# Optimization experiments

Hardware: AMD Instinct MI355X
Metric: run time of the kernel (lower is better)

The kernel has to match this reference:

```python
import jax, jax.numpy as jnp
import numpy as np

ALPHA = 0.02      # LeakyReLU negative slope
N_GRAPHS = 128    # number of graphs in the batch (global_mean_pool segments)
NEG_INF = jnp.float32(-9e15)


def _gat_head(x, mask, W, a1, a2):
    # One GraphAttentionLayer (no dropout: eval mode).
    Wh = x @ W                                   # [N, h]
    f1 = Wh @ a1                                 # [N] = a[:h] . Wh_i
    f2 = Wh @ a2                                 # [N] = a[h:] . Wh_j
    e = jax.nn.leaky_relu(f1[:, None] + f2[None, :], negative_slope=ALPHA)  # [N, N]
    e = jnp.where(mask, e, NEG_INF)              # adjacency-masked logits
    att = jax.nn.softmax(e, axis=-1)             # row-wise over neighbors
    return att @ Wh                              # [N, h]


def reference(x, edge_index, batch, W_heads, a1_heads, a2_heads,
              W_out, a1_out, a2_out, W1, b1, W2, b2):
    N = x.shape[0]
    # adj[src, dst] = 1 via scatter, exactly as the torch code
    adj = jnp.zeros((N, N), dtype=jnp.float32).at[edge_index[0], edge_index[1]].set(1.0)
    mask = adj > 0
    # multi-head GAT, heads vmapped: [H, N, h]
    heads = jax.vmap(_gat_head, in_axes=(None, None, 0, 0, 0))(
        x, mask, W_heads, a1_heads, a2_heads)
    heads = jax.nn.elu(heads)                    # concat=True applies elu per head
    h = jnp.transpose(heads, (1, 0, 2)).reshape(N, -1)   # concat -> [N, H*h]
    out = jax.nn.elu(_gat_head(h, mask, W_out, a1_out, a2_out))  # out_att + outer elu
    # global mean pool over graphs
    seg_sum = jax.ops.segment_sum(out, batch, num_segments=N_GRAPHS)
    counts = jax.ops.segment_sum(jnp.ones((N,), jnp.float32), batch, num_segments=N_GRAPHS)
    pooled = seg_sum / jnp.maximum(counts, 1.0)[:, None]          # [G, att_out]
    # MLP head
    hid = jax.nn.relu(pooled @ W1 + b1)
    return hid @ W2 + b2                                          # [G, nout]


def setup_inputs() -> dict:
    key = jax.random.key(0)
    ks = jax.random.split(key, 12)
    N, F, H, HID, OUT, MLP, NOUT, E = 2048, 300, 20, 600, 1000, 1000, 768, 32768
    s = 0.05
    return {
        "x": jax.random.normal(ks[0], (N, F), jnp.float32),
        "edge_index": jax.random.randint(ks[1], (2, E), 0, N),
        "batch": jnp.sort(jax.random.randint(ks[2], (N,), 0, N_GRAPHS)),
        "W_heads": jax.random.normal(ks[3], (H, F, HID), jnp.float32) * s,
        "a1_heads": jax.random.normal(ks[4], (H, HID), jnp.float32) * s,
        "a2_heads": jax.random.normal(ks[5], (H, HID), jnp.float32) * s,
        "W_out": jax.random.normal(ks[6], (H * HID, OUT), jnp.float32) * 0.01,
        "a1_out": jax.random.normal(ks[7], (OUT,), jnp.float32) * s,
        "a2_out": jax.random.normal(ks[8], (OUT,), jnp.float32) * s,
        "W1": jax.random.normal(ks[9], (OUT, MLP), jnp.float32) * 0.03,
        "b1": jnp.zeros((MLP,), jnp.float32),
        "W2": jax.random.normal(ks[10], (MLP, NOUT), jnp.float32) * 0.03,
        "b2": jnp.zeros((NOUT,), jnp.float32),
    }
```

## Files before the change

kernel.cpp:

```cpp
#include <hip/hip_runtime.h>
#include <math.h>

#define NN   2048
#define FF   300
#define FP   320
#define NH   20
#define HHID 600
#define HP   640
#define HCAT (NH * HHID)
#define DOUT 1000
#define NPAD 1024
#define MLPD 1000
#define NOUTD 768
#define NE   32768
#define NG   128
#define CAP  160
#define KSPL 6
#define KCH  2016
#define PVC  16
#define PVR  16
#define PVU  47
#define PVHALF 750

typedef __attribute__((ext_vector_type(8))) short short8;
typedef __attribute__((ext_vector_type(4))) float f32x4;

__device__ __forceinline__ unsigned short f2bf(float f) {
  unsigned int u = __float_as_uint(f);
  u += 0x7fffu + ((u >> 16) & 1u);
  return (unsigned short)(u >> 16);
}
__device__ __forceinline__ float bf2f(unsigned short u) {
  return __uint_as_float(((unsigned int)u) << 16);
}
__device__ __forceinline__ void st_out(float* p, float v) { *p = v; }
__device__ __forceinline__ void st_out(unsigned short* p, float v) { *p = f2bf(v); }


__global__ void zero_words(unsigned int* __restrict__ p, int n) {
  int i = blockIdx.x * blockDim.x + threadIdx.x;
  int stride = gridDim.x * blockDim.x;
  for (; i < n; i += stride) p[i] = 0u;
}

__global__ void scatter_mask(const int* __restrict__ ei, unsigned char* __restrict__ mask) {
  int e = blockIdx.x * blockDim.x + threadIdx.x;
  if (e < NE) {
    int s = ei[e], d = ei[NE + e];
    mask[(size_t)s * NN + d] = 1;
  }
}

__global__ void build_csr(const unsigned char* __restrict__ mask,
                          int* __restrict__ nbr, int* __restrict__ deg) {
  int wave = threadIdx.x >> 6, lane = threadIdx.x & 63;
  int i = blockIdx.x * 4 + wave;
  if (i >= NN) return;
  const unsigned* roww = (const unsigned*)(mask + (size_t)i * NN);
  int cnt = 0;
  for (int c0 = 0; c0 < NN; c0 += 256) {
    unsigned word = roww[(c0 >> 2) + lane];
#pragma unroll
    for (int b = 0; b < 4; b++) {
      bool p = ((word >> (8 * b)) & 0xffu) != 0u;
      unsigned long long bal = __ballot(p);
      if (p) {
        int pos = cnt + (int)__popcll(bal & ((1ull << lane) - 1ull));
        if (pos < CAP) nbr[(size_t)i * CAP + pos] = c0 + lane * 4 + b;
      }
      cnt += (int)__popcll(bal);
    }
  }
  if (lane == 0) deg[i] = cnt < CAP ? cnt : CAP;
}


__global__ void w12_kernel(const float* __restrict__ W, const float* __restrict__ a1,
                           const float* __restrict__ a2,
                           float* __restrict__ w1, float* __restrict__ w2) {
  int k = blockIdx.x, hd = blockIdx.y, lane = threadIdx.x;
  const float* r = W + ((size_t)hd * FF + k) * HHID;
  const float* A1 = a1 + (size_t)hd * HHID;
  const float* A2 = a2 + (size_t)hd * HHID;
  float s1 = 0.f, s2 = 0.f;
  for (int c = lane; c < HHID; c += 64) {
    float w = r[c];
    s1 += w * A1[c];
    s2 += w * A2[c];
  }
  for (int off = 32; off; off >>= 1) {
    s1 += __shfl_down(s1, off);
    s2 += __shfl_down(s2, off);
  }
  if (lane == 0) { w1[(size_t)hd * FF + k] = s1; w2[(size_t)hd * FF + k] = s2; }
}

__global__ __launch_bounds__(256)
void f12x_kernel(const float* __restrict__ x, const float* __restrict__ w1,
                 const float* __restrict__ w2,
                 float* __restrict__ f1, float* __restrict__ f2) {
  __shared__ float xr[FF];
  int i = blockIdx.x, t = threadIdx.x;
  for (int c = t; c < FF; c += 256) xr[c] = x[(size_t)i * FF + c];
  __syncthreads();
  if (t < 2 * NH) {
    int hd = t >> 1;
    const float* wv = ((t & 1) ? w2 : w1) + (size_t)hd * FF;
    float s = 0.f;
    for (int k = 0; k < FF; k++) s += xr[k] * wv[k];
    ((t & 1) ? f2 : f1)[(size_t)hd * NN + i] = s;
  }
}

__global__ __launch_bounds__(256)
void csa_kernel(const float* __restrict__ xsum, const float* __restrict__ W,
                float* __restrict__ csa) {
  __shared__ float xs[FF];
  int hd = blockIdx.y, t = threadIdx.x;
  for (int k = t; k < FF; k += 256) xs[k] = xsum[k];
  __syncthreads();
  int c = blockIdx.x * 256 + t;
  if (c >= HHID) return;
  const float* Wp = W + (size_t)hd * FF * HHID + c;
  float s = 0.f;
  for (int k = 0; k < FF; k++) s += xs[k] * Wp[(size_t)k * HHID];
  csa[(size_t)hd * HHID + c] = s;
}


__global__ void f12_kernel(const float* __restrict__ Wh, int ldw, int h,
                           const float* __restrict__ a1, const float* __restrict__ a2,
                           int astride,
                           float* __restrict__ f1, float* __restrict__ f2) {
  int i = blockIdx.x, hd = blockIdx.y;
  int lane = threadIdx.x;
  const float* r = Wh + (size_t)i * ldw + (size_t)hd * h;
  const float* A1 = a1 + (size_t)hd * astride;
  const float* A2 = a2 + (size_t)hd * astride;
  float s1 = 0.f, s2 = 0.f;
  for (int c = lane; c < h; c += 64) {
    float w = r[c];
    s1 += w * A1[c];
    s2 += w * A2[c];
  }
  for (int off = 32; off; off >>= 1) {
    s1 += __shfl_down(s1, off);
    s2 += __shfl_down(s2, off);
  }
  if (lane == 0) { f1[(size_t)hd * NN + i] = s1; f2[(size_t)hd * NN + i] = s2; }
}

__global__ void f12_bf16(const unsigned short* __restrict__ Wh, int ldw, int h,
                         const float* __restrict__ a1, const float* __restrict__ a2,
                         int astride,
                         float* __restrict__ f1, float* __restrict__ f2) {
  int i = blockIdx.x, hd = blockIdx.y;
  int lane = threadIdx.x;
  const unsigned short* r = Wh + (size_t)i * ldw + (size_t)hd * h;
  const float* A1 = a1 + (size_t)hd * astride;
  const float* A2 = a2 + (size_t)hd * astride;
  float s1 = 0.f, s2 = 0.f;
  for (int c8 = lane; c8 < h / 8; c8 += 64) {
    short8 v = *(const short8*)(r + (size_t)c8 * 8);
#pragma unroll
    for (int j = 0; j < 8; j++) {
      float w = bf2f((unsigned short)v[j]);
      s1 += w * A1[c8 * 8 + j];
      s2 += w * A2[c8 * 8 + j];
    }
  }
  for (int off = 32; off; off >>= 1) {
    s1 += __shfl_down(s1, off);
    s2 += __shfl_down(s2, off);
  }
  if (lane == 0) { f1[(size_t)hd * NN + i] = s1; f2[(size_t)hd * NN + i] = s2; }
}

__global__ void colsum_kernel(const float* __restrict__ Wh, int ldw, int h,
                              float* __restrict__ cs) {
  int hd = blockIdx.y;
  int c = blockIdx.x * blockDim.x + threadIdx.x;
  if (c >= h) return;
  size_t off = (size_t)hd * h + c;
  float s = 0.f;
  for (int i = 0; i < NN; i++) s += Wh[(size_t)i * ldw + off];
  cs[(size_t)hd * h + c] = s;
}

__global__ void colsum_at_bf16(const unsigned short* __restrict__ Wh, int ld, int width,
                               float* __restrict__ cs) {
  int c = blockIdx.x * blockDim.x + threadIdx.x;
  if (c >= width) return;
  int r0 = blockIdx.y * 64;
  float s = 0.f;
  for (int i = r0; i < r0 + 64; i++) s += bf2f(Wh[(size_t)i * ld + c]);
  atomicAdd(&cs[c], s);
}

__global__ void colsum_at_f32(const float* __restrict__ Wh, int ld, int width,
                              float* __restrict__ cs) {
  int c = blockIdx.x * blockDim.x + threadIdx.x;
  if (c >= width) return;
  int r0 = blockIdx.y * 64;
  float s = 0.f;
  for (int i = r0; i < r0 + 64; i++) s += Wh[(size_t)i * ld + c];
  atomicAdd(&cs[c], s);
}


template <typename OT>
__global__ __launch_bounds__(256)
void spmm_att(const float* __restrict__ Wh, int ldw, int h,
              const float* __restrict__ f1, const float* __restrict__ f2,
              const int* __restrict__ nbr, const int* __restrict__ deg,
              const float* __restrict__ cs,
              OT* __restrict__ outp, int ldo) {
  __shared__ float att[CAP];
  __shared__ int   nb[CAP];
  __shared__ float red[256];
  int i = blockIdx.x, hd = blockIdx.y;
  int t = threadIdx.x;
  int d = deg[i];
  size_t hoff = (size_t)hd * h;
  if (d > 0) {
    float fi = f1[(size_t)hd * NN + i];
    const float* F2 = f2 + (size_t)hd * NN;
    float lmax = -INFINITY;
    for (int k = t; k < d; k += 256) {
      int j = nbr[(size_t)i * CAP + k];
      nb[k] = j;
      float e = fi + F2[j];
      e = e > 0.f ? e : 0.02f * e;
      att[k] = e;
      lmax = fmaxf(lmax, e);
    }
    red[t] = lmax; __syncthreads();
    for (int s = 128; s; s >>= 1) { if (t < s) red[t] = fmaxf(red[t], red[t + s]); __syncthreads(); }
    float m = red[0]; __syncthreads();
    float ls = 0.f;
    for (int k = t; k < d; k += 256) { float p = expf(att[k] - m); att[k] = p; ls += p; }
    red[t] = ls; __syncthreads();
    for (int s = 128; s; s >>= 1) { if (t < s) red[t] += red[t + s]; __syncthreads(); }
    float inv = 1.0f / red[0]; __syncthreads();
    for (int k = t; k < d; k += 256) att[k] *= inv;
    __syncthreads();
    for (int c = t; c < h; c += 256) {
      float s = 0.f;
      for (int k = 0; k < d; k++) s += att[k] * Wh[(size_t)nb[k] * ldw + hoff + c];
      s = s > 0.f ? s : (expf(s) - 1.0f);
      st_out(&outp[(size_t)i * ldo + hoff + c], s);
    }
  } else {
    const float inv = 1.0f / (float)NN;
    for (int c = t; c < h; c += 256) {
      float s = cs[hoff + c] * inv;
      s = s > 0.f ? s : (expf(s) - 1.0f);
      st_out(&outp[(size_t)i * ldo + hoff + c], s);
    }
  }
}

__global__ __launch_bounds__(256)
void att_pre(const float* __restrict__ f1, const float* __restrict__ f2,
             const int* __restrict__ nbr, const int* __restrict__ deg,
             float* __restrict__ att_c) {
  __shared__ int   nb_sh[CAP];
  __shared__ float att_sh[4][CAP];
  int i = blockIdx.x;
  int t = threadIdx.x, w = t >> 6, lane = t & 63;
  int hd = blockIdx.y * 4 + w;
  int d = deg[i];
  if (d == 0) return;
  for (int k = t; k < d; k += 256) nb_sh[k] = nbr[(size_t)i * CAP + k];
  __syncthreads();
  float fi = f1[(size_t)hd * NN + i];
  const float* F2 = f2 + (size_t)hd * NN;
  float lmax = -INFINITY;
  for (int k = lane; k < d; k += 64) {
    float e = fi + F2[nb_sh[k]];
    e = e > 0.f ? e : 0.02f * e;
    att_sh[w][k] = e;
    lmax = fmaxf(lmax, e);
  }
  for (int off = 32; off; off >>= 1) lmax = fmaxf(lmax, __shfl_xor(lmax, off));
  float ls = 0.f;
  for (int k = lane; k < d; k += 64) {
    float p = expf(att_sh[w][k] - lmax);
    att_sh[w][k] = p; ls += p;
  }
  for (int off = 32; off; off >>= 1) ls += __shfl_xor(ls, off);
  float inv = 1.0f / ls;
  float* ao = att_c + ((size_t)i * NH + hd) * CAP;
  for (int k = lane; k < d; k += 64) ao[k] = att_sh[w][k] * inv;
}

__global__ __launch_bounds__(256)
void spmm_pv(const unsigned short* __restrict__ Whb,
             const float* __restrict__ att_c,
             const int* __restrict__ nbr, const int* __restrict__ deg,
             const float* __restrict__ cs,
             unsigned short* __restrict__ outp,
             int ubase) {
  __shared__ int nb_sh[PVR][CAP];
  __shared__ int d_sh[PVR];
  int t = threadIdx.x;
  int r0 = blockIdx.y * PVR;
  int u0 = ubase + blockIdx.x * PVU;
  int ulim = ubase + PVHALF;
  int nu = (u0 + PVU <= ulim) ? PVU : (ulim - u0);
  if (t < PVR) d_sh[t] = deg[r0 + t];
  for (int q = t; q < PVR * CAP; q += 256) {
    int r = q / CAP, k = q - r * CAP;
    nb_sh[r][k] = nbr[(size_t)(r0 + r) * CAP + k];
  }
  __syncthreads();
  const float invn = 1.0f / (float)NN;
  int total = PVR * nu;
  for (int q = t; q < total; q += 256) {
    int r = q / nu, u = q - r * nu;
    int i = r0 + r;
    int gu = u0 + u;
    int hd = gu / (HHID / 8);
    int d = d_sh[r];
    const unsigned short* base = Whb + (size_t)gu * 8;
    unsigned short o8[8];
    if (d > 0) {
      const float* av = att_c + ((size_t)i * NH + hd) * CAP;
      float a8[8] = {};
      for (int k = 0; k < d; k++) {
        float a = av[k];
        short8 v = *(const short8*)(base + (size_t)nb_sh[r][k] * HCAT);
#pragma unroll
        for (int j = 0; j < 8; j++) a8[j] += a * bf2f((unsigned short)v[j]);
      }
#pragma unroll
      for (int j = 0; j < 8; j++) {
        float s = a8[j];
        s = s > 0.f ? s : (expf(s) - 1.0f);
        o8[j] = f2bf(s);
      }
    } else {
#pragma unroll
      for (int j = 0; j < 8; j++) {
        float s = cs[(size_t)gu * 8 + j] * invn;
        s = s > 0.f ? s : (expf(s) - 1.0f);
        o8[j] = f2bf(s);
      }
    }
    *(short8*)(outp + (size_t)i * HCAT + (size_t)gu * 8) = *(const short8*)o8;
  }
}

__global__ __launch_bounds__(128)
void spmm_att_o(const unsigned short* __restrict__ Wh,
                const float* __restrict__ f1, const float* __restrict__ f2,
                const int* __restrict__ nbr, const int* __restrict__ deg,
                const float* __restrict__ cs,
                float* __restrict__ outp) {
  __shared__ int   nb_sh[CAP];
  __shared__ float att_sh[CAP];
  __shared__ float red[128];
  int i = blockIdx.x, t = threadIdx.x;
  int d = deg[i];
  if (d > 0) {
    float fi = f1[i];
    float lmax = -INFINITY;
    for (int k = t; k < d; k += 128) {
      int j = nbr[(size_t)i * CAP + k];
      nb_sh[k] = j;
      float e = fi + f2[j];
      e = e > 0.f ? e : 0.02f * e;
      att_sh[k] = e;
      lmax = fmaxf(lmax, e);
    }
    red[t] = lmax; __syncthreads();
    for (int s = 64; s; s >>= 1) { if (t < s) red[t] = fmaxf(red[t], red[t + s]); __syncthreads(); }
    float m = red[0]; __syncthreads();
    float ls = 0.f;
    for (int k = t; k < d; k += 128) { float p = expf(att_sh[k] - m); att_sh[k] = p; ls += p; }
    red[t] = ls; __syncthreads();
    for (int s = 64; s; s >>= 1) { if (t < s) red[t] += red[t + s]; __syncthreads(); }
    float inv = 1.0f / red[0]; __syncthreads();
    for (int k = t; k < d; k += 128) att_sh[k] *= inv;
    __syncthreads();
    for (int cc = t; cc < DOUT / 8; cc += 128) {
      float a8[8] = {};
      const unsigned short* base = Wh + (size_t)cc * 8;
      for (int k = 0; k < d; k++) {
        float av = att_sh[k];
        short8 v = *(const short8*)(base + (size_t)nb_sh[k] * DOUT);
#pragma unroll
      for (int j = 0; j < 8; j++)
          a8[j] += av * bf2f((unsigned short)v[j]);
      }
      float o[8];
#pragma unroll
      for (int j = 0; j < 8; j++) {
        float s = a8[j];
        o[j] = s > 0.f ? s : (expf(s) - 1.0f);
      }
      *(float4*)(outp + (size_t)i * DOUT + (size_t)cc * 8)     = make_float4(o[0], o[1], o[2], o[3]);
      *(float4*)(outp + (size_t)i * DOUT + (size_t)cc * 8 + 4) = make_float4(o[4], o[5], o[6], o[7]);
    }
  } else {
    const float invn = 1.0f / (float)NN;
    for (int c = t; c < DOUT; c += 128) {
      float s = cs[c] * invn;
      outp[(size_t)i * DOUT + c] = s > 0.f ? s : (expf(s) - 1.0f);
    }
  }
}


__global__ void conv_x_bf16(const float* __restrict__ x, unsigned short* __restrict__ xb) {
  int i = blockIdx.x, t = threadIdx.x;
  float v = (t < FF) ? x[(size_t)i * FF + t] : 0.0f;
  xb[(size_t)i * FP + t] = f2bf(v);
}

__global__ void convT_gen(const float* __restrict__ W, unsigned short* __restrict__ Wt,
                          int K, int N, int ldw, long wz, int ldt, long tz) {
  __shared__ float tile[32][33];
  const float* Wp = W + (size_t)blockIdx.z * wz;
  unsigned short* Tp = Wt + (size_t)blockIdx.z * tz;
  int k0 = blockIdx.x * 32, n0 = blockIdx.y * 32;
  int tx = threadIdx.x, ty = threadIdx.y;
#pragma unroll
  for (int r = ty; r < 32; r += 8) {
    int kk = k0 + r, n = n0 + tx;
    tile[r][tx] = (kk < K && n < N) ? Wp[(size_t)kk * ldw + n] : 0.0f;
  }
  __syncthreads();
#pragma unroll
  for (int r = ty; r < 32; r += 8) {
    Tp[(size_t)(n0 + r) * ldt + k0 + tx] = f2bf(tile[tx][r]);
  }
}

__global__ void conv_f2b(const float* __restrict__ in, unsigned short* __restrict__ out, int n) {
  int i = blockIdx.x * blockDim.x + threadIdx.x;
  int stride = gridDim.x * blockDim.x;
  for (; i < n; i += stride) out[i] = f2bf(in[i]);
}

template <int LDA, int LDB, int LDC, int NREAL, int KCHUNK, int KTOT, int SWZ, typename OT>
__global__ __launch_bounds__(256)
void gemm_bf16_t(const unsigned short* __restrict__ A, long az,
                 const unsigned short* __restrict__ Bt, long bz,
                 OT* __restrict__ C, long cz) {
  __shared__ __align__(16) unsigned short As[128 * 32];
  __shared__ __align__(16) unsigned short Bs[128 * 32];
  int bx = blockIdx.x, by = blockIdx.y, bz_ = blockIdx.z;
  if (SWZ) {
    int gx = gridDim.x, gy = gridDim.y;
    int nwg = gx * gy * gridDim.z;
    int lin = bx + gx * (by + gy * bz_);
    int q = nwg >> 3;
    int lin2 = (lin & 7) * q + (lin >> 3);
    bx = lin2 % gx; by = (lin2 / gx) % gy; bz_ = lin2 / (gx * gy);
  }
  const int z = bz_;
  A  += (size_t)z * az;
  Bt += (size_t)z * bz;
  C  += (size_t)z * cz;
  int ks, ke;
  if (KCHUNK > 0) {
    ks = z * KCHUNK;
    ke = (ks + KCHUNK < KTOT) ? (ks + KCHUNK) : KTOT;
  } else {
    ks = 0; ke = KTOT;
  }
  const int t = threadIdx.x;
  const int w = t >> 6, lane = t & 63;
  const int m0 = by * 128, n0 = bx * 128;
  const int c0 = t, c1 = t + 256;
  const int ra0 = c0 >> 2, ca0 = (c0 & 3) * 8;
  const int ra1 = c1 >> 2, ca1 = (c1 & 3) * 8;
  const unsigned short* gA0 = A + (size_t)(m0 + ra0) * LDA + ca0;
  const unsigned short* gA1 = A + (size_t)(m0 + ra1) * LDA + ca1;
  const unsigned short* gB0 = Bt + (size_t)(n0 + ra0) * LDB + ca0;
  const unsigned short* gB1 = Bt + (size_t)(n0 + ra1) * LDB + ca1;
  unsigned short* lA0 = As + (size_t)w * 512;
  unsigned short* lA1 = As + (size_t)(4 + w) * 512;
  unsigned short* lB0 = Bs + (size_t)w * 512;
  unsigned short* lB1 = Bs + (size_t)(4 + w) * 512;
  const int wm = (w >> 1) * 64, wn = (w & 1) * 64;
  const int arow = lane & 15, acol = (lane >> 4) * 8;
  f32x4 acc[4][4] = {};
  for (int k = ks; k < ke; k += 32) {
    __builtin_amdgcn_global_load_lds((const __attribute__((address_space(1))) void*)(gA0 + k),
                                     (__attribute__((address_space(3))) void*)(lA0), 16, 0, 0);
    __builtin_amdgcn_global_load_lds((const __attribute__((address_space(1))) void*)(gA1 + k),
                                     (__attribute__((address_space(3))) void*)(lA1), 16, 0, 0);
    __builtin_amdgcn_global_load_lds((const __attribute__((address_space(1))) void*)(gB0 + k),
                                     (__attribute__((address_space(3))) void*)(lB0), 16, 0, 0);
    __builtin_amdgcn_global_load_lds((const __attribute__((address_space(1))) void*)(gB1 + k),
                                     (__attribute__((address_space(3))) void*)(lB1), 16, 0, 0);
    __syncthreads();
    short8 a[4], b[4];
#pragma unroll
    for (int i = 0; i < 4; i++)
      a[i] = *(const short8*)&As[(wm + i * 16 + arow) * 32 + acol];
#pragma unroll
    for (int j = 0; j < 4; j++)
      b[j] = *(const short8*)&Bs[(wn + j * 16 + arow) * 32 + acol];
#pragma unroll
    for (int i = 0; i < 4; i++)
#pragma unroll
      for (int j = 0; j < 4; j++)
        acc[i][j] = __builtin_amdgcn_mfma_f32_16x16x32_bf16(a[i], b[j], acc[i][j], 0, 0, 0);
    __syncthreads();
  }
  const int crow = (lane >> 4) * 4, ccol = lane & 15;
#pragma unroll
  for (int i = 0; i < 4; i++)
#pragma unroll
    for (int j = 0; j < 4; j++) {
      int gc = n0 + wn + j * 16 + ccol;
      if (gc < NREAL) {
#pragma unroll
        for (int r = 0; r < 4; r++)
          st_out(&C[(size_t)(m0 + wm + i * 16 + crow + r) * LDC + gc], acc[i][j][r]);
      }
    }
}

__global__ void addn_kernel(const float* __restrict__ p, unsigned short* __restrict__ ob) {
  const int n = NN * DOUT;
  int i = blockIdx.x * blockDim.x + threadIdx.x;
  int stride = gridDim.x * blockDim.x;
  for (; i < n; i += stride) {
    float v = 0.f;
#pragma unroll
    for (int z = 0; z < KSPL; z++) v += p[(size_t)z * n + i];
    ob[i] = f2bf(v);
  }
}

template <int K, int KS>
__global__ __launch_bounds__(256)
void gemm_thin(const float* __restrict__ A, const float* __restrict__ B,
               float* __restrict__ P, int N) {
  constexpr int KC = K / KS;
  __shared__ float Ash[128][KC + 3];
  int t = threadIdx.x;
  int tx = t & 63, ty = t >> 6;
  int n0 = blockIdx.x * 64, kz = blockIdx.y;
  int ks = kz * KC;
  for (int idx = t; idx < 128 * KC; idx += 256) {
    int r = idx / KC, c = idx - r * KC;
    Ash[r][c] = A[(size_t)r * K + ks + c];
  }
  __syncthreads();
  int nn = n0 + tx; if (nn > N - 1) nn = N - 1;
  const float* Bp = B + (size_t)ks * N + nn;
  int m0 = ty * 32;
  float acc[32] = {};
  for (int k4 = 0; k4 < KC / 4; k4++) {
    int k = k4 * 4;
    float w0 = Bp[(size_t)(k + 0) * N];
    float w1 = Bp[(size_t)(k + 1) * N];
    float w2 = Bp[(size_t)(k + 2) * N];
    float w3 = Bp[(size_t)(k + 3) * N];
#pragma unroll
    for (int mm = 0; mm < 32; mm++) {
      float4 a = *(const float4*)&Ash[m0 + mm][k];
      acc[mm] += a.x * w0 + a.y * w1 + a.z * w2 + a.w * w3;
    }
  }
#pragma unroll
  for (int k = (KC / 4) * 4; k < KC; k++) {
    float w0 = Bp[(size_t)k * N];
#pragma unroll
    for (int mm = 0; mm < 32; mm++) acc[mm] += Ash[m0 + mm][k] * w0;
  }
  if (n0 + tx < N) {
    float* Pp = P + (size_t)kz * 128 * N;
#pragma unroll
    for (int mm = 0; mm < 32; mm++)
      Pp[(size_t)(m0 + mm) * N + n0 + tx] = acc[mm];
  }
}

template <int N, int KS, int EPI>
__global__ void thin_reduce(const float* __restrict__ P, const float* __restrict__ bias,
                            float* __restrict__ C) {
  int i = blockIdx.x * blockDim.x + threadIdx.x;
  const int total = 128 * N;
  if (i >= total) return;
  int n = i % N;
  float v = 0.f;
#pragma unroll
  for (int z = 0; z < KS; z++) v += P[(size_t)z * total + i];
  v += bias[n];
  if (EPI == 2) v = v > 0.f ? v : 0.f;
  C[i] = v;
}

template <int BM_, int BN_, int EPI>
__global__ __launch_bounds__(256)
void gemm_t(const float* __restrict__ A, const float* __restrict__ B,
            float* __restrict__ C, const float* __restrict__ bias,
            int M, int N, int K, int lda, int ldb, int ldc, int accum,
            long bz, long cz) {
  constexpr int MR = BM_ / 16, NR = BN_ / 16;
  __shared__ float As[16][BM_ + 4];
  __shared__ float Bs[16][BN_ + 4];
  const float* Bp = B + (size_t)blockIdx.z * bz;
  float* Cp = C + (size_t)blockIdx.z * cz;
  int tx = threadIdx.x, ty = threadIdx.y;
  int tid = ty * 16 + tx;
  int m0 = blockIdx.y * BM_, n0 = blockIdx.x * BN_;
  float acc[MR][NR] = {};
  for (int k0 = 0; k0 < K; k0 += 16) {
#pragma unroll
    for (int p = 0; p < BM_ / 64; p++) {
      int id = tid + p * 256;
      int r = id >> 2, c4 = (id & 3) * 4;
      int gm = m0 + r;
      float v[4];
      if (gm < M && k0 + c4 + 3 < K) {
        const float4 t4 = *(const float4*)&A[(size_t)gm * lda + k0 + c4];
        v[0] = t4.x; v[1] = t4.y; v[2] = t4.z; v[3] = t4.w;
      } else {
#pragma unroll
        for (int q = 0; q < 4; q++) {
          int gk = k0 + c4 + q;
          v[q] = (gm < M && gk < K) ? A[(size_t)gm * lda + gk] : 0.0f;
        }
      }
#pragma unroll
      for (int q = 0; q < 4; q++) As[c4 + q][r] = v[q];
    }
#pragma unroll
    for (int p = 0; p < BN_ / 64; p++) {
      int id = tid + p * 256;
      int r = id / (BN_ / 4), c4 = (id % (BN_ / 4)) * 4;
      int gk = k0 + r, gn = n0 + c4;
      float v[4];
      if (gk < K && gn + 3 < N) {
        const float4 t4 = *(const float4*)&Bp[(size_t)gk * ldb + gn];
        v[0] = t4.x; v[1] = t4.y; v[2] = t4.z; v[3] = t4.w;
      } else {
#pragma unroll
        for (int q = 0; q < 4; q++)
          v[q] = (gk < K && gn + q < N) ? Bp[(size_t)gk * ldb + gn + q] : 0.0f;
      }
      *(float4*)&Bs[r][c4] = *(const float4*)v;
    }
    __syncthreads();
#pragma unroll
    for (int kk = 0; kk < 16; kk++) {
      float a[MR], b[NR];
#pragma unroll
      for (int q = 0; q < MR / 4; q++)
        *(float4*)&a[q * 4] = *(const float4*)&As[kk][ty * MR + q * 4];
#pragma unroll
      for (int q = 0; q < NR / 4; q++)
        *(float4*)&b[q * 4] = *(const float4*)&Bs[kk][tx * NR + q * 4];
#pragma unroll
      for (int i = 0; i < MR; i++)
#pragma unroll
        for (int j = 0; j < NR; j++) acc[i][j] += a[i] * b[j];
    }
    __syncthreads();
  }
#pragma unroll
  for (int i = 0; i < MR; i++) {
    int gm = m0 + ty * MR + i;
    if (gm >= M) continue;
#pragma unroll
    for (int j = 0; j < NR; j++) {
      int gn = n0 + tx * NR + j;
      if (gn >= N) continue;
      float r = acc[i][j];
      if (accum) r += Cp[(size_t)gm * ldc + gn];
      if (EPI == 2) { r += bias[gn]; r = r > 0.f ? r : 0.f; }
      else if (EPI == 3) { r += bias[gn]; }
      Cp[(size_t)gm * ldc + gn] = r;
    }
  }
}


__global__ void pool_prep(const int* __restrict__ batch, int* __restrict__ startg, int* __restrict__ cntg) {
  int n = blockIdx.x * blockDim.x + threadIdx.x;
  if (n >= NN) return;
  int b = batch[n];
  if (n == 0 || batch[n - 1] != b) startg[b] = n;
  atomicAdd(&cntg[b], 1);
}

__global__ void pool_kernel(const float* __restrict__ outb,
                            const int* __restrict__ startg, const int* __restrict__ cntg,
                            float* __restrict__ pooled) {
  int g = blockIdx.x, t = threadIdx.x;
  int st = startg[g], c = cntg[g];
  for (int ch = t; ch < DOUT; ch += 256) {
    float s = 0.f;
    for (int k = 0; k < c; k++) s += outb[(size_t)(st + k) * DOUT + ch];
    pooled[(size_t)g * DOUT + ch] = s / (float)(c > 0 ? c : 1);
  }
}


static inline int cdiv(int a, int b) { return (a + b - 1) / b; }

extern "C" void kernel_launch(void* const* d_in, const int* in_sizes, int n_in,
                              void* d_out, int out_size, void* d_ws, size_t ws_size,
                              hipStream_t stream) {
  const float* x        = (const float*)d_in[0];
  const int*   ei       = (const int*)d_in[1];
  const int*   batch    = (const int*)d_in[2];
  const float* W_heads  = (const float*)d_in[3];
  const float* a1_heads = (const float*)d_in[4];
  const float* a2_heads = (const float*)d_in[5];
  const float* W_out    = (const float*)d_in[6];
  const float* a1_out   = (const float*)d_in[7];
  const float* a2_out   = (const float*)d_in[8];
  const float* W1       = (const float*)d_in[9];
  const float* b1       = (const float*)d_in[10];
  const float* W2       = (const float*)d_in[11];
  const float* b2       = (const float*)d_in[12];
  float* outd = (float*)d_out;
  (void)in_sizes; (void)n_in; (void)out_size;

  char* w = (char*)d_ws;
  size_t off = 0;
  auto alloc = [&](size_t bytes) {
    void* p = w + off;
    off += (bytes + 255) & ~(size_t)255;
    return p;
  };
  auto al = [](size_t b) { return (b + 255) & ~(size_t)255; };

  unsigned char* mask = (unsigned char*)alloc((size_t)NN * NN);
  int*   nbr    = (int*)alloc((size_t)NN * CAP * 4);
  int*   deg    = (int*)alloc((size_t)NN * 4);
  float* acc    = (float*)alloc((size_t)NN * DOUT * 4);
  unsigned short* accb = (unsigned short*)alloc((size_t)NN * DOUT * 2);
  float* outb   = (float*)alloc((size_t)NN * DOUT * 4);
  float* f1o    = (float*)alloc((size_t)NN * 4);
  float* f2o    = (float*)alloc((size_t)NN * 4);
  float* cso    = (float*)alloc((size_t)DOUT * 4);
  float* pooled = (float*)alloc((size_t)NG * DOUT * 4);
  float* hid    = (float*)alloc((size_t)NG * MLPD * 4);
  int*   startg = (int*)alloc((size_t)NG * 4);
  int*   cntg   = (int*)alloc((size_t)NG * 4);
  size_t off_common = off;

  size_t need_batched = off_common
      + al((size_t)NN * HCAT * 2)
      + al((size_t)NN * HCAT * 2)
      + al((size_t)NPAD * HCAT * 2)
      + al((size_t)NN * FP * 2)
      + al((size_t)NH * HP * FP * 2)
      + al((size_t)NN * NH * CAP * 4)
      + al((size_t)NH * NN * 4) * 2
      + al((size_t)NH * HHID * 4)
      + al((size_t)NH * FF * 4) * 2
      + al((size_t)FF * 4);
  bool batched = ws_size >= need_batched;

  zero_words<<<4096, 256, 0, stream>>>((unsigned int*)mask, NN * NN / 4);
  scatter_mask<<<cdiv(NE, 256), 256, 0, stream>>>(ei, mask);
  build_csr<<<NN / 4, 256, 0, stream>>>(mask, nbr, deg);

  if (batched) {
    unsigned short* Whb   = (unsigned short*)alloc((size_t)NN * HCAT * 2);
    unsigned short* hcatb = (unsigned short*)alloc((size_t)NN * HCAT * 2);
    unsigned short* Wt    = (unsigned short*)alloc((size_t)NPAD * HCAT * 2);
    unsigned short* xb    = (unsigned short*)alloc((size_t)NN * FP * 2);
    unsigned short* Wth   = (unsigned short*)alloc((size_t)NH * HP * FP * 2);
    float* att_c  = (float*)alloc((size_t)NN * NH * CAP * 4);
    float* f1a    = (float*)alloc((size_t)NH * NN * 4);
    float* f2a    = (float*)alloc((size_t)NH * NN * 4);
    float* csa    = (float*)alloc((size_t)NH * HHID * 4);
    float* w1b    = (float*)alloc((size_t)NH * FF * 4);
    float* w2b    = (float*)alloc((size_t)NH * FF * 4);
    float* xsum   = (float*)alloc((size_t)FF * 4);
    float* partC = (float*)Whb;

    conv_x_bf16<<<NN, FP, 0, stream>>>(x, xb);
    convT_gen<<<dim3(FP / 32, HP / 32, NH), dim3(32, 8), 0, stream>>>(
        W_heads, Wth, FF, HHID, HHID, (long)FF * HHID, FP, (long)HP * FP);
    gemm_bf16_t<FP, FP, HCAT, HHID, 0, FP, 0, unsigned short>
        <<<dim3(HP / 128, NN / 128, NH), 256, 0, stream>>>(
        xb, 0L, Wth, (long)HP * FP, Whb, (long)HHID);
    w12_kernel<<<dim3(FF, NH), 64, 0, stream>>>(W_heads, a1_heads, a2_heads, w1b, w2b);
    f12x_kernel<<<NN, 256, 0, stream>>>(x, w1b, w2b, f1a, f2a);
    zero_words<<<1, 256, 0, stream>>>((unsigned int*)xsum, FF);
    colsum_at_f32<<<dim3(cdiv(FF, 256), NN / 64), 256, 0, stream>>>(x, FF, FF, xsum);
    csa_kernel<<<dim3(cdiv(HHID, 256), NH), 256, 0, stream>>>(xsum, W_heads, csa);
    convT_gen<<<dim3(HCAT / 32, NPAD / 32, 1), dim3(32, 8), 0, stream>>>(
        W_out, Wt, HCAT, DOUT, DOUT, 0L, HCAT, 0L);
    att_pre<<<dim3(NN, NH / 4), 256, 0, stream>>>(f1a, f2a, nbr, deg, att_c);
    spmm_pv<<<dim3(PVC, NN / PVR), 256, 0, stream>>>(Whb, att_c, nbr, deg, csa, hcatb, 0);
    spmm_pv<<<dim3(PVC, NN / PVR), 256, 0, stream>>>(Whb, att_c, nbr, deg, csa, hcatb, PVHALF);
    gemm_bf16_t<HCAT, HCAT, DOUT, DOUT, KCH, HCAT, 1, float>
        <<<dim3(NPAD / 128, NN / 128, KSPL), 256, 0, stream>>>(
        hcatb, 0L, Wt, 0L, partC, (long)NN * DOUT);
    addn_kernel<<<2048, 256, 0, stream>>>(partC, accb);
    f12_bf16<<<dim3(NN, 1), 64, 0, stream>>>(accb, DOUT, DOUT, a1_out, a2_out, 0, f1o, f2o);
    zero_words<<<1, 256, 0, stream>>>((unsigned int*)cso, DOUT);
    colsum_at_bf16<<<dim3(cdiv(DOUT, 256), NN / 64), 256, 0, stream>>>(accb, DOUT, DOUT, cso);
    spmm_att_o<<<dim3(NN), 128, 0, stream>>>(accb, f1o, f2o, nbr, deg, cso, outb);
  } else {
    float* Wh   = (float*)alloc((size_t)NN * HHID * 4);
    float* hout = (float*)alloc((size_t)NN * HHID * 4);
    float* f1   = (float*)alloc((size_t)NN * 4);
    float* f2   = (float*)alloc((size_t)NN * 4);
    float* cs   = (float*)alloc((size_t)HHID * 4);
    zero_words<<<8000, 256, 0, stream>>>((unsigned int*)acc, NN * DOUT);
    for (int hd = 0; hd < NH; hd++) {
      gemm_t<64, 64, 0><<<dim3(cdiv(HHID, 64), cdiv(NN, 64), 1), dim3(16, 16), 0, stream>>>(
          x, W_heads + (size_t)hd * FF * HHID, Wh, nullptr,
          NN, HHID, FF, FF, HHID, HHID, 0, 0L, 0L);
      f12_kernel<<<dim3(NN, 1), 64, 0, stream>>>(Wh, HHID, HHID,
          a1_heads + (size_t)hd * HHID, a2_heads + (size_t)hd * HHID, 0, f1, f2);
      colsum_kernel<<<dim3(cdiv(HHID, 256), 1), 256, 0, stream>>>(Wh, HHID, HHID, cs);
      spmm_att<float><<<dim3(NN, 1), 256, 0, stream>>>(Wh, HHID, HHID, f1, f2,
                                                       nbr, deg, cs, hout, HHID);
      gemm_t<64, 64, 0><<<dim3(cdiv(DOUT, 64), cdiv(NN, 64), 1), dim3(16, 16), 0, stream>>>(
          hout, W_out + (size_t)hd * HHID * DOUT, acc, nullptr,
          NN, DOUT, HHID, HHID, DOUT, DOUT, 1, 0L, 0L);
    }
    conv_f2b<<<2048, 256, 0, stream>>>(acc, accb, NN * DOUT);
    f12_kernel<<<dim3(NN, 1), 64, 0, stream>>>(acc, DOUT, DOUT, a1_out, a2_out, 0, f1o, f2o);
    zero_words<<<1, 256, 0, stream>>>((unsigned int*)cso, DOUT);
    colsum_at_f32<<<dim3(cdiv(DOUT, 256), NN / 64), 256, 0, stream>>>(acc, DOUT, DOUT, cso);
    spmm_att_o<<<dim3(NN), 128, 0, stream>>>(accb, f1o, f2o, nbr, deg, cso, outb);
  }

  zero_words<<<1, 256, 0, stream>>>((unsigned int*)startg, NG * 2);
  pool_prep<<<NN / 256, 256, 0, stream>>>(batch, startg, cntg);
  pool_kernel<<<NG, 256, 0, stream>>>(outb, startg, cntg, pooled);

  float* mlpP = acc;
  gemm_thin<DOUT, 8><<<dim3(cdiv(MLPD, 64), 8), 256, 0, stream>>>(pooled, W1, mlpP, MLPD);
  thin_reduce<MLPD, 8, 2><<<cdiv(NG * MLPD, 256), 256, 0, stream>>>(mlpP, b1, hid);
  gemm_thin<MLPD, 8><<<dim3(cdiv(NOUTD, 64), 8), 256, 0, stream>>>(hid, W2, mlpP, NOUTD);
  thin_reduce<NOUTD, 8, 3><<<cdiv(NG * NOUTD, 256), 256, 0, stream>>>(mlpP, b2, outd);
}
```

Measured before the change: 390.9 us.

## Raise K-split to eight, split csa over K with atomics, merge spmm launches

After: 409.3 us. 1.05x slower.

```diff
diff --git a/kernel.cpp b/kernel.cpp
--- a/kernel.cpp
+++ b/kernel.cpp
@@ -15,12 +15,12 @@
 #define NE   32768
 #define NG   128
 #define CAP  160
-#define KSPL 6
-#define KCH  2016
+#define KSPL 8
+#define KSP0 6
+#define KCH  1504
 #define PVC  16
 #define PVR  16
-#define PVU  47
-#define PVHALF 750
+#define PVU  94
 
 typedef __attribute__((ext_vector_type(8))) short short8;
 typedef __attribute__((ext_vector_type(4))) float f32x4;
@@ -113,18 +113,20 @@
 }
 
 __global__ __launch_bounds__(256)
-void csa_kernel(const float* __restrict__ xsum, const float* __restrict__ W,
-                float* __restrict__ csa) {
-  __shared__ float xs[FF];
-  int hd = blockIdx.y, t = threadIdx.x;
-  for (int k = t; k < FF; k += 256) xs[k] = xsum[k];
+void csa_at(const float* __restrict__ xsum, const float* __restrict__ W,
+            float* __restrict__ csa) {
+  __shared__ float xs[60];
+  int hd = blockIdx.y, kz = blockIdx.z, t = threadIdx.x;
+  int k0 = kz * 60;
+  int nk = (k0 + 60 <= FF) ? 60 : (FF - k0);
+  if (t < nk) xs[t] = xsum[k0 + t];
   __syncthreads();
   int c = blockIdx.x * 256 + t;
   if (c >= HHID) return;
-  const float* Wp = W + (size_t)hd * FF * HHID + c;
+  const float* Wp = W + ((size_t)hd * FF + k0) * HHID + c;
   float s = 0.f;
-  for (int k = 0; k < FF; k++) s += xs[k] * Wp[(size_t)k * HHID];
-  csa[(size_t)hd * HHID + c] = s;
+  for (int k = 0; k < nk; k++) s += xs[k] * Wp[(size_t)k * HHID];
+  atomicAdd(&csa[(size_t)hd * HHID + c], s);
 }
 
 
@@ -299,15 +301,13 @@
              const float* __restrict__ att_c,
              const int* __restrict__ nbr, const int* __restrict__ deg,
              const float* __restrict__ cs,
-             unsigned short* __restrict__ outp,
-             int ubase) {
+             unsigned short* __restrict__ outp) {
   __shared__ int nb_sh[PVR][CAP];
   __shared__ int d_sh[PVR];
   int t = threadIdx.x;
   int r0 = blockIdx.y * PVR;
-  int u0 = ubase + blockIdx.x * PVU;
-  int ulim = ubase + PVHALF;
-  int nu = (u0 + PVU <= ulim) ? PVU : (ulim - u0);
+  int u0 = blockIdx.x * PVU;
+  int nu = (u0 + PVU <= HCAT / 8) ? PVU : (HCAT / 8 - u0);
   if (t < PVR) d_sh[t] = deg[r0 + t];
   for (int q = t; q < PVR * CAP; q += 256) {
     int r = q / CAP, k = q - r * CAP;
@@ -447,7 +447,7 @@
 __global__ __launch_bounds__(256)
 void gemm_bf16_t(const unsigned short* __restrict__ A, long az,
                  const unsigned short* __restrict__ Bt, long bz,
-                 OT* __restrict__ C, long cz) {
+                 OT* __restrict__ C0, OT* __restrict__ C1, int zsplit, long cz) {
   __shared__ __align__(16) unsigned short As[128 * 32];
   __shared__ __align__(16) unsigned short Bs[128 * 32];
   int bx = blockIdx.x, by = blockIdx.y, bz_ = blockIdx.z;
@@ -462,7 +462,7 @@
   const int z = bz_;
   A  += (size_t)z * az;
   Bt += (size_t)z * bz;
-  C  += (size_t)z * cz;
+  OT* C = (z < zsplit) ? (C0 + (size_t)z * cz) : (C1 + (size_t)(z - zsplit) * cz);
   int ks, ke;
   if (KCHUNK > 0) {
     ks = z * KCHUNK;
@@ -525,14 +525,17 @@
     }
 }
 
-__global__ void addn_kernel(const float* __restrict__ p, unsigned short* __restrict__ ob) {
+__global__ void addn_kernel(const float* __restrict__ p0, const float* __restrict__ p1,
+                            unsigned short* __restrict__ ob) {
   const int n = NN * DOUT;
   int i = blockIdx.x * blockDim.x + threadIdx.x;
   int stride = gridDim.x * blockDim.x;
   for (; i < n; i += stride) {
     float v = 0.f;
 #pragma unroll
-    for (int z = 0; z < KSPL; z++) v += p[(size_t)z * n + i];
+    for (int z = 0; z < KSP0; z++) v += p0[(size_t)z * n + i];
+#pragma unroll
+    for (int z = 0; z < KSPL - KSP0; z++) v += p1[(size_t)z * n + i];
     ob[i] = f2bf(v);
   }
 }
@@ -779,28 +782,29 @@
     float* w1b    = (float*)alloc((size_t)NH * FF * 4);
     float* w2b    = (float*)alloc((size_t)NH * FF * 4);
     float* xsum   = (float*)alloc((size_t)FF * 4);
-    float* partC = (float*)Whb;
+    float* partC0 = (float*)Whb;
+    float* partC1 = att_c;
 
     conv_x_bf16<<<NN, FP, 0, stream>>>(x, xb);
     convT_gen<<<dim3(FP / 32, HP / 32, NH), dim3(32, 8), 0, stream>>>(
         W_heads, Wth, FF, HHID, HHID, (long)FF * HHID, FP, (long)HP * FP);
-    gemm_bf16_t<FP, FP, HCAT, HHID, 0, FP, 0, unsigned short>
+    gemm_bf16_t<FP, FP, HCAT, HHID, 0, FP, 1, unsigned short>
         <<<dim3(HP / 128, NN / 128, NH), 256, 0, stream>>>(
-        xb, 0L, Wth, (long)HP * FP, Whb, (long)HHID);
+        xb, 0L, Wth, (long)HP * FP, Whb, Whb, NH, (long)HHID);
     w12_kernel<<<dim3(FF, NH), 64, 0, stream>>>(W_heads, a1_heads, a2_heads, w1b, w2b);
     f12x_kernel<<<NN, 256, 0, stream>>>(x, w1b, w2b, f1a, f2a);
     zero_words<<<1, 256, 0, stream>>>((unsigned int*)xsum, FF);
     colsum_at_f32<<<dim3(cdiv(FF, 256), NN / 64), 256, 0, stream>>>(x, FF, FF, xsum);
-    csa_kernel<<<dim3(cdiv(HHID, 256), NH), 256, 0, stream>>>(xsum, W_heads, csa);
+    zero_words<<<12, 256, 0, stream>>>((unsigned int*)csa, NH * HHID);
+    csa_at<<<dim3(cdiv(HHID, 256), NH, 5), 256, 0, stream>>>(xsum, W_heads, csa);
     convT_gen<<<dim3(HCAT / 32, NPAD / 32, 1), dim3(32, 8), 0, stream>>>(
         W_out, Wt, HCAT, DOUT, DOUT, 0L, HCAT, 0L);
     att_pre<<<dim3(NN, NH / 4), 256, 0, stream>>>(f1a, f2a, nbr, deg, att_c);
-    spmm_pv<<<dim3(PVC, NN / PVR), 256, 0, stream>>>(Whb, att_c, nbr, deg, csa, hcatb, 0);
-    spmm_pv<<<dim3(PVC, NN / PVR), 256, 0, stream>>>(Whb, att_c, nbr, deg, csa, hcatb, PVHALF);
+    spmm_pv<<<dim3(PVC, NN / PVR), 256, 0, stream>>>(Whb, att_c, nbr, deg, csa, hcatb);
     gemm_bf16_t<HCAT, HCAT, DOUT, DOUT, KCH, HCAT, 1, float>
         <<<dim3(NPAD / 128, NN / 128, KSPL), 256, 0, stream>>>(
-        hcatb, 0L, Wt, 0L, partC, (long)NN * DOUT);
-    addn_kernel<<<2048, 256, 0, stream>>>(partC, accb);
+        hcatb, 0L, Wt, 0L, partC0, partC1, KSP0, (long)NN * DOUT);
+    addn_kernel<<<2048, 256, 0, stream>>>(partC0, partC1, accb);
     f12_bf16<<<dim3(NN, 1), 64, 0, stream>>>(accb, DOUT, DOUT, a1_out, a2_out, 0, f1o, f2o);
     zero_words<<<1, 256, 0, stream>>>((unsigned int*)cso, DOUT);
     colsum_at_bf16<<<dim3(cdiv(DOUT, 256), NN / 64), 256, 0, stream>>>(accb, DOUT, DOUT, cso);
```
